# Kernel optimization log

Measured on AMD Instinct MI355X. Metric: run time of the kernel, lower is better.

## Reference

```python
import jax, jax.numpy as jnp
import numpy as np

N_STREAMS = 4
DIM = 256
TMAX = 20
RMS_EPS = 1e-05
SK_EPS = 1e-08


def sinkhorn_knopp(logits):
    # logits: [B, T, n, n]; tmax fixed iterations of row/col normalization
    x = logits.astype(jnp.float32)
    x = x - jnp.max(x, axis=(-2, -1), keepdims=True)
    x = jnp.exp(x)
    for _ in range(TMAX):
        x = x / (jnp.sum(x, axis=-2, keepdims=True) + SK_EPS)
        x = x / (jnp.sum(x, axis=-1, keepdims=True) + SK_EPS)
    return x.astype(logits.dtype)


def setup_inputs() -> dict:
    key = jax.random.key(0)
    ks = jax.random.split(key, 5)
    B, T, n, C = 8, 4096, N_STREAMS, DIM
    nc = n * C
    x_streams = jax.random.normal(ks[0], (B, T, n, C), dtype=jnp.float32)
    scale = jnp.ones((nc,), dtype=jnp.float32)
    lim = 1.0 / np.sqrt(nc)
    w_pre = jax.random.uniform(ks[1], (n, nc), minval=-lim, maxval=lim, dtype=jnp.float32)
    w_post = jax.random.uniform(ks[2], (n, nc), minval=-lim, maxval=lim, dtype=jnp.float32)
    w_res = jax.random.uniform(ks[3], (n * n, nc), minval=-lim, maxval=lim, dtype=jnp.float32)
    return {
        "x_streams": x_streams,
        "scale": scale,
        "w_pre": w_pre,
        "w_post": w_post,
        "w_res": w_res,
        "alpha_pre": jnp.float32(0.01),
        "alpha_post": jnp.float32(0.01),
        "alpha_res": jnp.float32(0.01),
        "b_pre": jnp.zeros((n,), dtype=jnp.float32),
        "b_post": jnp.zeros((n,), dtype=jnp.float32),
        "b_res": jnp.zeros((n * n,), dtype=jnp.float32),
    }


def reference(x_streams, scale, w_pre, w_post, w_res,
              alpha_pre, alpha_post, alpha_res, b_pre, b_post, b_res):
    B, T, n, C = x_streams.shape
    x_flat = x_streams.reshape(B, T, n * C)
    # RMSNorm over flattened stream dim
    rms = jnp.mean(x_flat * x_flat, axis=-1, keepdims=True)
    x_norm = x_flat * jax.lax.rsqrt(rms + RMS_EPS) * scale
    # routing projections (Linear with no bias == x @ W.T)
    h_pre = jax.nn.sigmoid(alpha_pre * (x_norm @ w_pre.T) + b_pre)          # [B,T,n]
    h_post = 2.0 * jax.nn.sigmoid(alpha_post * (x_norm @ w_post.T) + b_post)  # [B,T,n]
    h_res = (alpha_res * (x_norm @ w_res.T) + b_res).reshape(B, T, n, n)
    h_res = sinkhorn_knopp(h_res)
    # mixing
    x_in = jnp.einsum('btn,btnc->btc', h_pre, x_streams)   # pre-mix (residual = Identity)
    y = x_in
    resmix = jnp.einsum('btij,btjc->btic', h_res, x_streams)
    addy = h_post[..., None] * y[..., None, :]
    return resmix + addy
```

## Files before the change

### kernel.cpp

```cpp
#include <hip/hip_runtime.h>
#include <math.h>

#define G 16

__device__ __forceinline__ float sigmoidf_(float s) {
    return 1.0f / (1.0f + __expf(-s));
}

__global__ __launch_bounds__(256, 2)
void fused_route_mix(const float* __restrict__ x,
                     const float* __restrict__ scale,
                     const float* __restrict__ w_pre,
                     const float* __restrict__ w_post,
                     const float* __restrict__ w_res,
                     const float* __restrict__ ap_p,
                     const float* __restrict__ apo_p,
                     const float* __restrict__ ar_p,
                     const float* __restrict__ b_pre,
                     const float* __restrict__ b_post,
                     const float* __restrict__ b_res,
                     float* __restrict__ out,
                     int rounds)
{
    __shared__ __align__(16) float xs[G * 1024];
    __shared__ float hraw[G * 24];
    __shared__ float sslds[G];
    __shared__ __align__(16) float Mlds[G * 16];

    const int t = threadIdx.x;
    const int w = t >> 6;
    const int l = t & 63;

    float wreg[6][16];
    {
        float scl[16];
        #pragma unroll
        for (int m = 0; m < 16; ++m) scl[m] = scale[l + 64 * m];
        #pragma unroll
        for (int rr = 0; rr < 6; ++rr) {
            const int k = 6 * w + rr;
            const float* wp = (k < 4) ? (w_pre + (size_t)k * 1024)
                            : (k < 8) ? (w_post + (size_t)(k - 4) * 1024)
                                      : (w_res + (size_t)(k - 8) * 1024);
            #pragma unroll
            for (int m = 0; m < 16; ++m)
                wreg[rr][m] = wp[l + 64 * m] * scl[m];
        }
    }

    const float a_pre = ap_p[0], a_post = apo_p[0], a_res = ar_p[0];

    for (int r = blockIdx.x; r < rounds; r += gridDim.x) {
        const size_t base = (size_t)r * (G * 1024);

        const float4* __restrict__ xg = (const float4*)(x + base);
        float4* xs4 = (float4*)xs;
        #pragma unroll
        for (int i = 0; i < G; ++i)
            xs4[i * 256 + t] = xg[i * 256 + t];
        __syncthreads();

        for (int i = 0; i < G; ++i) {
            float p0 = 0.f, p1 = 0.f, p2 = 0.f, p3 = 0.f, p4 = 0.f, p5 = 0.f;
            float ssp = 0.f;
            const float* xi = xs + i * 1024 + l;
            #pragma unroll
            for (int m = 0; m < 16; ++m) {
                const float xv = xi[64 * m];
                p0 = fmaf(xv, wreg[0][m], p0);
                p1 = fmaf(xv, wreg[1][m], p1);
                p2 = fmaf(xv, wreg[2][m], p2);
                p3 = fmaf(xv, wreg[3][m], p3);
                p4 = fmaf(xv, wreg[4][m], p4);
                p5 = fmaf(xv, wreg[5][m], p5);
                if (w == 0) ssp = fmaf(xv, xv, ssp);
            }
            #pragma unroll
            for (int mask = 1; mask < 64; mask <<= 1) {
                p0 += __shfl_xor(p0, mask);
                p1 += __shfl_xor(p1, mask);
                p2 += __shfl_xor(p2, mask);
                p3 += __shfl_xor(p3, mask);
                p4 += __shfl_xor(p4, mask);
                p5 += __shfl_xor(p5, mask);
                if (w == 0) ssp += __shfl_xor(ssp, mask);
            }
            if (l == 0) {
                float* h = hraw + i * 24 + 6 * w;
                h[0] = p0; h[1] = p1; h[2] = p2;
                h[3] = p3; h[4] = p4; h[5] = p5;
                if (w == 0) sslds[i] = ssp;
            }
        }
        __syncthreads();

        if (t < G) {
            const int tk = t;
            const float inv = rsqrtf(sslds[tk] * (1.0f / 1024.0f) + 1e-5f);
            float hr[24];
            #pragma unroll
            for (int k = 0; k < 24; ++k) hr[k] = hraw[tk * 24 + k];

            float hpre[4], hpost[4];
            #pragma unroll
            for (int j = 0; j < 4; ++j)
                hpre[j] = sigmoidf_(fmaf(a_pre * inv, hr[j], b_pre[j]));
            #pragma unroll
            for (int i = 0; i < 4; ++i)
                hpost[i] = 2.0f * sigmoidf_(fmaf(a_post * inv, hr[4 + i], b_post[i]));

            float K[4][4];
            float mx = -1e30f;
            #pragma unroll
            for (int i = 0; i < 4; ++i) {
                #pragma unroll
                for (int j = 0; j < 4; ++j) {
                    const float vv = fmaf(a_res * inv, hr[8 + 4 * i + j], b_res[4 * i + j]);
                    K[i][j] = vv;
                    mx = fmaxf(mx, vv);
                }
            }
            #pragma unroll
            for (int i = 0; i < 4; ++i)
                #pragma unroll
                for (int j = 0; j < 4; ++j)
                    K[i][j] = __expf(K[i][j] - mx);

            float u[4] = {1.f, 1.f, 1.f, 1.f};
            float v[4] = {1.f, 1.f, 1.f, 1.f};
            for (int it = 0; it < 20; ++it) {
                #pragma unroll
                for (int j = 0; j < 4; ++j) {
                    const float S = u[0] * K[0][j] + u[1] * K[1][j]
                                  + u[2] * K[2][j] + u[3] * K[3][j];
                    v[j] = v[j] * __builtin_amdgcn_rcpf(fmaf(v[j], S, 1e-8f));
                }
                #pragma unroll
                for (int i = 0; i < 4; ++i) {
                    const float T = K[i][0] * v[0] + K[i][1] * v[1]
                                  + K[i][2] * v[2] + K[i][3] * v[3];
                    u[i] = u[i] * __builtin_amdgcn_rcpf(fmaf(u[i], T, 1e-8f));
                }
            }
            #pragma unroll
            for (int i = 0; i < 4; ++i)
                #pragma unroll
                for (int j = 0; j < 4; ++j)
                    Mlds[tk * 16 + 4 * i + j] =
                        fmaf(u[i] * K[i][j], v[j], hpost[i] * hpre[j]);
        }
        __syncthreads();

        for (int i = 0; i < G; ++i) {
            const float4 m4 = ((const float4*)Mlds)[i * 4 + w];
            const float4* xt = xs4 + i * 256;
            const float4 a0 = xt[0 * 64 + l];
            const float4 a1 = xt[1 * 64 + l];
            const float4 a2 = xt[2 * 64 + l];
            const float4 a3 = xt[3 * 64 + l];
            float4 o;
            o.x = m4.x * a0.x + m4.y * a1.x + m4.z * a2.x + m4.w * a3.x;
            o.y = m4.x * a0.y + m4.y * a1.y + m4.z * a2.y + m4.w * a3.y;
            o.z = m4.x * a0.z + m4.y * a1.z + m4.z * a2.z + m4.w * a3.z;
            o.w = m4.x * a0.w + m4.y * a1.w + m4.z * a2.w + m4.w * a3.w;
            ((float4*)(out + base))[i * 256 + w * 64 + l] = o;
        }
        __syncthreads();
    }
}

extern "C" void kernel_launch(void* const* d_in, const int* in_sizes, int n_in,
                              void* d_out, int out_size, void* d_ws, size_t ws_size,
                              hipStream_t stream) {
    const float* x      = (const float*)d_in[0];
    const float* scale  = (const float*)d_in[1];
    const float* w_pre  = (const float*)d_in[2];
    const float* w_post = (const float*)d_in[3];
    const float* w_res  = (const float*)d_in[4];
    const float* a_pre  = (const float*)d_in[5];
    const float* a_post = (const float*)d_in[6];
    const float* a_res  = (const float*)d_in[7];
    const float* b_pre  = (const float*)d_in[8];
    const float* b_post = (const float*)d_in[9];
    const float* b_res  = (const float*)d_in[10];
    float* out = (float*)d_out;

    const int tokens = in_sizes[0] / 1024;
    const int rounds = tokens / G;
    const int grid = rounds < 1024 ? rounds : 1024;

    fused_route_mix<<<grid, 256, 0, stream>>>(
        x, scale, w_pre, w_post, w_res,
        a_pre, a_post, a_res, b_pre, b_post, b_res,
        out, rounds);
}
```

Baseline: 293.0 us.

## Halve token group, raise occupancy, and use DPP transposed reductions

Cuts the per-block token group from 16 to 8, which halves LDS use, and raises launch bounds so more blocks can be resident per CU. Replaces the seven independent 64-lane shuffle butterflies with a DPP-based transposed reduction, where lanes specialise on different partial sums so fewer cross-lane operations are needed. It also switches weight, scale and LDS reads to float4 vectors with a matching element mapping. The trade-off is more grid rounds and more register pressure under the tighter launch bound.

```diff
diff --git a/kernel.cpp b/kernel.cpp
--- a/kernel.cpp
+++ b/kernel.cpp
@@ -1,13 +1,19 @@
 #include <hip/hip_runtime.h>
 #include <math.h>
 
-#define G 16
+#define G 8
 
 __device__ __forceinline__ float sigmoidf_(float s) {
     return 1.0f / (1.0f + __expf(-s));
 }
 
-__global__ __launch_bounds__(256, 2)
+template <int CTRL>
+__device__ __forceinline__ float dpp_add(float v) {
+    int m = __builtin_amdgcn_update_dpp(0, __float_as_int(v), CTRL, 0xF, 0xF, true);
+    return v + __int_as_float(m);
+}
+
+__global__ __launch_bounds__(256, 4)
 void fused_route_mix(const float* __restrict__ x,
                      const float* __restrict__ scale,
                      const float* __restrict__ w_pre,
@@ -33,64 +39,85 @@
 
     float wreg[6][16];
     {
-        float scl[16];
+        const float4* sc4 = (const float4*)scale;
+        float4 scl[4];
         #pragma unroll
-        for (int m = 0; m < 16; ++m) scl[m] = scale[l + 64 * m];
+        for (int m = 0; m < 4; ++m) scl[m] = sc4[64 * m + l];
         #pragma unroll
         for (int rr = 0; rr < 6; ++rr) {
             const int k = 6 * w + rr;
             const float* wp = (k < 4) ? (w_pre + (size_t)k * 1024)
                             : (k < 8) ? (w_post + (size_t)(k - 4) * 1024)
                                       : (w_res + (size_t)(k - 8) * 1024);
-            #pragma unroll
-            for (int m = 0; m < 16; ++m)
-                wreg[rr][m] = wp[l + 64 * m] * scl[m];
+            const float4* wp4 = (const float4*)wp;
+            #pragma unroll
+            for (int m = 0; m < 4; ++m) {
+                const float4 v = wp4[64 * m + l];
+                wreg[rr][m * 4 + 0] = v.x * scl[m].x;
+                wreg[rr][m * 4 + 1] = v.y * scl[m].y;
+                wreg[rr][m * 4 + 2] = v.z * scl[m].z;
+                wreg[rr][m * 4 + 3] = v.w * scl[m].w;
+            }
         }
     }
 
     const float a_pre = ap_p[0], a_post = apo_p[0], a_res = ar_p[0];
+    float4* xs4 = (float4*)xs;
 
     for (int r = blockIdx.x; r < rounds; r += gridDim.x) {
         const size_t base = (size_t)r * (G * 1024);
 
-        const float4* __restrict__ xg = (const float4*)(x + base);
-        float4* xs4 = (float4*)xs;
+        const float4* __restrict__ xg4 = (const float4*)(x + base);
         #pragma unroll
         for (int i = 0; i < G; ++i)
-            xs4[i * 256 + t] = xg[i * 256 + t];
+            xs4[i * 256 + t] = xg4[i * 256 + t];
         __syncthreads();
 
         for (int i = 0; i < G; ++i) {
             float p0 = 0.f, p1 = 0.f, p2 = 0.f, p3 = 0.f, p4 = 0.f, p5 = 0.f;
-            float ssp = 0.f;
-            const float* xi = xs + i * 1024 + l;
-            #pragma unroll
-            for (int m = 0; m < 16; ++m) {
-                const float xv = xi[64 * m];
-                p0 = fmaf(xv, wreg[0][m], p0);
-                p1 = fmaf(xv, wreg[1][m], p1);
-                p2 = fmaf(xv, wreg[2][m], p2);
-                p3 = fmaf(xv, wreg[3][m], p3);
-                p4 = fmaf(xv, wreg[4][m], p4);
-                p5 = fmaf(xv, wreg[5][m], p5);
-                if (w == 0) ssp = fmaf(xv, xv, ssp);
+            float ssa = 0.f;
+            const float4* xi4 = xs4 + i * 256 + l;
+            #pragma unroll
+            for (int m = 0; m < 4; ++m) {
+                const float4 xv = xi4[m * 64];
+                const float xe[4] = {xv.x, xv.y, xv.z, xv.w};
+                #pragma unroll
+                for (int e = 0; e < 4; ++e) {
+                    const float xf = xe[e];
+                    const int c = m * 4 + e;
+                    p0 = fmaf(xf, wreg[0][c], p0);
+                    p1 = fmaf(xf, wreg[1][c], p1);
+                    p2 = fmaf(xf, wreg[2][c], p2);
+                    p3 = fmaf(xf, wreg[3][c], p3);
+                    p4 = fmaf(xf, wreg[4][c], p4);
+                    p5 = fmaf(xf, wreg[5][c], p5);
+                    ssa = fmaf(xf, xf, ssa);
+                }
             }
-            #pragma unroll
-            for (int mask = 1; mask < 64; mask <<= 1) {
-                p0 += __shfl_xor(p0, mask);
-                p1 += __shfl_xor(p1, mask);
-                p2 += __shfl_xor(p2, mask);
-                p3 += __shfl_xor(p3, mask);
-                p4 += __shfl_xor(p4, mask);
-                p5 += __shfl_xor(p5, mask);
-                if (w == 0) ssp += __shfl_xor(ssp, mask);
-            }
-            if (l == 0) {
-                float* h = hraw + i * 24 + 6 * w;
-                h[0] = p0; h[1] = p1; h[2] = p2;
-                h[3] = p3; h[4] = p4; h[5] = p5;
-                if (w == 0) sslds[i] = ssp;
-            }
+            const float a0 = dpp_add<0xB1>(p0), a1 = dpp_add<0xB1>(p1);
+            const float a2 = dpp_add<0xB1>(p2), a3 = dpp_add<0xB1>(p3);
+            const float a4 = dpp_add<0xB1>(p4), a5 = dpp_add<0xB1>(p5);
+            const float a6 = dpp_add<0xB1>(ssa);
+            const bool b0 = l & 1;
+            const float q0 = b0 ? a1 : a0;
+            const float q1 = b0 ? a3 : a2;
+            const float q2 = b0 ? a5 : a4;
+            const float q3 = b0 ? 0.0f : a6;
+            const float c0 = dpp_add<0x4E>(q0), c1 = dpp_add<0x4E>(q1);
+            const float c2 = dpp_add<0x4E>(q2), c3 = dpp_add<0x4E>(q3);
+            const bool b1 = l & 2;
+            const float r0 = b1 ? c1 : c0;
+            const float r1 = b1 ? c3 : c2;
+            const float d0 = r0 + __shfl_xor(r0, 4);
+            const float d1 = r1 + __shfl_xor(r1, 4);
+            float s = (l & 4) ? d1 : d0;
+            s = dpp_add<0x128>(s);
+            s += __shfl_xor(s, 16);
+            s += __shfl_xor(s, 32);
+
+            const int k = l & 7;
+            if (k < 6 && l < 8) hraw[i * 24 + 6 * w + k] = s;
+            if (w == 0 && l == 6) sslds[i] = s;
         }
         __syncthreads();
 
@@ -99,7 +126,7 @@
             const float inv = rsqrtf(sslds[tk] * (1.0f / 1024.0f) + 1e-5f);
             float hr[24];
             #pragma unroll
-            for (int k = 0; k < 24; ++k) hr[k] = hraw[tk * 24 + k];
+            for (int k2 = 0; k2 < 24; ++k2) hr[k2] = hraw[tk * 24 + k2];
 
             float hpre[4], hpost[4];
             #pragma unroll
@@ -112,14 +139,13 @@
             float K[4][4];
             float mx = -1e30f;
             #pragma unroll
-            for (int i = 0; i < 4; ++i) {
+            for (int i = 0; i < 4; ++i)
                 #pragma unroll
                 for (int j = 0; j < 4; ++j) {
                     const float vv = fmaf(a_res * inv, hr[8 + 4 * i + j], b_res[4 * i + j]);
                     K[i][j] = vv;
                     mx = fmaxf(mx, vv);
                 }
-            }
             #pragma unroll
             for (int i = 0; i < 4; ++i)
                 #pragma unroll
```

Measured after the change: 392.8 us. 34.1% more time.
